# Performance work log

Measured on AMD Instinct MI355X. Metric: run time of the kernel, lower is better.

The kernel has to match this reference:

```python
import jax, jax.numpy as jnp
import numpy as np


def _knn_idx(xyz_bn3, k):
    # dist[b,i,j] = ||x_i - x_j||^2 over the point cloud.
    # Faithful to the source: torch.topk defaults to largest=True, so the
    # k+1 LARGEST distances are selected and index 0 (the farthest) is dropped.
    sq = jnp.sum(xyz_bn3 ** 2, axis=-1)  # [b, n]
    dist = sq[:, :, None] + sq[:, None, :] - 2.0 * jnp.einsum('bic,bjc->bij', xyz_bn3, xyz_bn3)
    _, idx = jax.lax.top_k(dist, k + 1)  # largest, sorted descending -> [b, n, k+1]
    return idx[:, :, 1:]  # drop slot 0, keep k neighbors -> [b, n, k]


def setup_inputs() -> dict:
    key = jax.random.key(0)
    B, N, C, K, NB = 8, 4096, 128, 20, 3
    ks = jax.random.split(key, 4)
    scale = 1.0 / np.sqrt(C).astype(np.float32)
    xyz = jax.random.normal(ks[0], (B, 3, N), jnp.float32)
    points = jax.random.normal(ks[1], (B, C, N), jnp.float32)
    W1 = jax.random.normal(ks[2], (NB, C, C), jnp.float32) * scale  # convs[2i] 1x1 kernels
    b1 = jnp.zeros((NB, C), jnp.float32)
    W2 = jax.random.normal(ks[3], (NB, C, C), jnp.float32) * scale  # convs[2i+1] 1x1 kernels
    b2 = jnp.zeros((NB, C), jnp.float32)
    return {"xyz": xyz, "points": points, "W1": W1, "b1": b1, "W2": W2, "b2": b2, "k": K}


def reference(xyz, points, W1, b1, W2, b2, k):
    # xyz: [b, 3, n]; points: [b, C, n]; W1/W2: [n_blocks, C, C]; b1/b2: [n_blocks, C]
    n_blocks = W1.shape[0]
    xyz_bn3 = jnp.transpose(xyz, (0, 2, 1))  # [b, n, 3]
    for i in range(n_blocks):
        shortcut = points
        p = jax.nn.leaky_relu(points, 0.01)  # elementwise, layout [b, C, n]
        # center branch: 1x1 conv == per-point linear
        center = jnp.einsum('oc,bcn->bon', W1[i], p) + b1[i][None, :, None]  # [b, C, n]
        if i == 0:
            idx = _knn_idx(xyz_bn3, k)  # [b, n, k], int32
            # grouping_operation gather: grouped[b,c,n,j] = p[b,c, idx[b,n,j]]
            grouped = jax.vmap(lambda pb, ib: pb[:, ib])(p, idx)  # [b, C, n, k]
            gnn = jnp.einsum('oc,bcnk->bonk', W2[i], grouped) + b2[i][None, :, None, None]
            # mean over concat([center(1 slot), gnn(k slots)], slot axis)
            agg = (center + jnp.sum(gnn, axis=-1)) / (k + 1)
        else:
            # later blocks: grouped_points is just the center point itself (K=1)
            gnn = jnp.einsum('oc,bcn->bon', W2[i], p) + b2[i][None, :, None]
            agg = (center + gnn) * 0.5
        points = agg + shortcut
    return points
```

## Files before the change

### kernel.cpp

```cpp
#include <hip/hip_runtime.h>
#include <math.h>

#define B 8
#define N 4096
#define C 128
#define K 20
#define M (B*N)

__device__ __forceinline__ float lrelu(float x) { return x > 0.f ? x : 0.01f * x; }

__global__ void prep_all(const float* __restrict__ xyz,
                         const float* __restrict__ W1, const float* __restrict__ b1,
                         const float* __restrict__ W2, const float* __restrict__ b2,
                         float4* __restrict__ xt, float* __restrict__ wt,
                         float* __restrict__ bias) {
    int blk = blockIdx.x;
    if (blk < 64) {
        int t = blk * 256 + threadIdx.x;
        int c = t >> 7, o = t & 127;
        int oc = o * C + c;
        wt[t]             = W1[oc] * (1.f / 21.f);
        wt[C * C + t]     = W2[oc] * (1.f / 21.f);
        wt[2 * C * C + t] = (W1[C * C + oc] + W2[C * C + oc]) * 0.5f;
        wt[3 * C * C + t] = (W1[2 * C * C + oc] + W2[2 * C * C + oc]) * 0.5f;
        if (t < C) {
            bias[t]         = (b1[t] + 20.f * b2[t]) * (1.f / 21.f);
            bias[C + t]     = (b1[C + t] + b2[C + t]) * 0.5f;
            bias[2 * C + t] = (b1[2 * C + t] + b2[2 * C + t]) * 0.5f;
        }
    } else {
        int t = (blk - 64) * 256 + threadIdx.x;
        int b = t >> 12, n = t & (N - 1);
        const float* p = xyz + (size_t)b * 3 * N;
        float x = p[n], y = p[N + n], z = p[2 * N + n];
        xt[t] = make_float4(x, y, z, x * x + y * y + z * z);
    }
}

__global__ __launch_bounds__(256) void transpose_rs(const float* __restrict__ in,
                                                    float* __restrict__ out, int R, int S) {
    __shared__ float tile[64][65];
    int b = blockIdx.z;
    int r0 = blockIdx.y * 64, s0 = blockIdx.x * 64;
    const float* pin = in + (size_t)b * R * S;
    float* pout = out + (size_t)b * R * S;
    int tr = threadIdx.x >> 4;
    int ts = (threadIdx.x & 15) << 2;
#pragma unroll
    for (int i = 0; i < 4; ++i) {
        int r = tr + i * 16;
        float4 v = *(const float4*)&pin[(size_t)(r0 + r) * S + s0 + ts];
        tile[r][ts + 0] = v.x; tile[r][ts + 1] = v.y;
        tile[r][ts + 2] = v.z; tile[r][ts + 3] = v.w;
    }
    __syncthreads();
#pragma unroll
    for (int i = 0; i < 4; ++i) {
        int s = tr + i * 16;
        float4 v = make_float4(tile[ts + 0][s], tile[ts + 1][s], tile[ts + 2][s], tile[ts + 3][s]);
        *(float4*)&pout[(size_t)(s0 + s) * R + r0 + ts] = v;
    }
}

__global__ __launch_bounds__(256, 4) void knn_kernel(const float4* __restrict__ xt,
                                                     int* __restrict__ idx) {
    __shared__ float maxred[4][4];
    __shared__ unsigned int wcnt[2][4][4];
    __shared__ unsigned int cnt[4];
    __shared__ unsigned long long cand[4][128];

    const int tid = threadIdx.x;
    const int wid = tid >> 6, lane = tid & 63;
    const int blk = blockIdx.x;
    const int b = blk >> 10;
    const int i0 = (blk & 1023) << 2;
    const float4* __restrict__ xb = xt + (size_t)b * N;

    float4 xi0 = xb[i0 + 0], xi1 = xb[i0 + 1], xi2 = xb[i0 + 2], xi3 = xb[i0 + 3];
    if (tid < 4) cnt[tid] = 0;

    float d[4][16];
    float mx0 = -1e30f, mx1 = -1e30f, mx2 = -1e30f, mx3 = -1e30f;
#pragma unroll
    for (int u = 0; u < 16; ++u) {
        float4 xj = xb[u * 256 + tid];
        float s0 = fmaf(xi0.x, xj.x, fmaf(xi0.y, xj.y, xi0.z * xj.z));
        float s1 = fmaf(xi1.x, xj.x, fmaf(xi1.y, xj.y, xi1.z * xj.z));
        float s2 = fmaf(xi2.x, xj.x, fmaf(xi2.y, xj.y, xi2.z * xj.z));
        float s3 = fmaf(xi3.x, xj.x, fmaf(xi3.y, xj.y, xi3.z * xj.z));
        float d0 = xi0.w + xj.w - 2.f * s0;
        float d1 = xi1.w + xj.w - 2.f * s1;
        float d2 = xi2.w + xj.w - 2.f * s2;
        float d3 = xi3.w + xj.w - 2.f * s3;
        d[0][u] = d0; d[1][u] = d1; d[2][u] = d2; d[3][u] = d3;
        mx0 = fmaxf(mx0, d0); mx1 = fmaxf(mx1, d1);
        mx2 = fmaxf(mx2, d2); mx3 = fmaxf(mx3, d3);
    }
#pragma unroll
    for (int off = 32; off; off >>= 1) {
        mx0 = fmaxf(mx0, __shfl_xor(mx0, off));
        mx1 = fmaxf(mx1, __shfl_xor(mx1, off));
        mx2 = fmaxf(mx2, __shfl_xor(mx2, off));
        mx3 = fmaxf(mx3, __shfl_xor(mx3, off));
    }
    if (lane == 0) {
        maxred[wid][0] = mx0; maxred[wid][1] = mx1;
        maxred[wid][2] = mx2; maxred[wid][3] = mx3;
    }
    __syncthreads();

    float lo[4] = {0.f, 0.f, 0.f, 0.f};
    float hi[4], thr[4];
    bool done[4] = {false, false, false, false};
#pragma unroll
    for (int r = 0; r < 4; ++r) {
        hi[r] = fmaxf(fmaxf(maxred[0][r], maxred[1][r]), fmaxf(maxred[2][r], maxred[3][r]));
        thr[r] = 0.f;
    }

    bool alldone = false;
    for (int it = 0; it < 24 && !alldone; ++it) {
        int p = it & 1;
#pragma unroll
        for (int r = 0; r < 4; ++r) {
            if (done[r]) continue;
            float t = 0.5f * (lo[r] + hi[r]);
            thr[r] = t;
            unsigned int cc = 0;
#pragma unroll
            for (int u = 0; u < 16; ++u)
                cc += (unsigned int)__popcll(__ballot(d[r][u] > t));
            if (lane == 0) wcnt[p][wid][r] = cc;
        }
        __syncthreads();
        alldone = true;
#pragma unroll
        for (int r = 0; r < 4; ++r) {
            if (done[r]) continue;
            unsigned int tot = wcnt[p][0][r] + wcnt[p][1][r] + wcnt[p][2][r] + wcnt[p][3][r];
            if (tot >= (unsigned)(K + 1) && tot <= 96u) done[r] = true;
            else if (tot > 96u) lo[r] = thr[r];
            else hi[r] = thr[r];
            if (!done[r]) alldone = false;
        }
    }
#pragma unroll
    for (int r = 0; r < 4; ++r) if (!done[r]) thr[r] = lo[r];

#pragma unroll
    for (int u = 0; u < 16; ++u) {
#pragma unroll
        for (int r = 0; r < 4; ++r) {
            bool pred = d[r][u] > thr[r];
            unsigned long long m = __ballot(pred);
            if (m) {
                unsigned int base = 0;
                if (lane == 0) base = atomicAdd(&cnt[r], (unsigned int)__popcll(m));
                base = (unsigned int)__shfl((int)base, 0);
                if (pred) {
                    unsigned int bel = __builtin_amdgcn_mbcnt_lo((unsigned int)m, 0u);
                    bel = __builtin_amdgcn_mbcnt_hi((unsigned int)(m >> 32), bel);
                    unsigned int pos = base + bel;
                    if (pos < 128u) {
                        unsigned int j = (unsigned int)(u * 256 + tid);
                        cand[r][pos] = ((unsigned long long)__float_as_uint(d[r][u]) << 32)
                                       | (unsigned int)(~j);
                    }
                }
            }
        }
    }
    __syncthreads();

    {
        int r = wid;
        int row = (b << 12) + i0 + r;
        unsigned int c = cnt[r]; if (c > 128u) c = 128u;
        if (c < (unsigned)(K + 1) && lane < K)
            idx[(size_t)row * K + lane] = (int)lane + 1;
        for (int s = lane; s < (int)c; s += 64) {
            unsigned long long my = cand[r][s];
            int rank = 0;
            for (int q = 0; q < (int)c; ++q) rank += (cand[r][q] > my) ? 1 : 0;
            if (rank >= 1 && rank <= K)
                idx[(size_t)row * K + (rank - 1)] = (int)(~(unsigned int)my);
        }
    }
}

__global__ __launch_bounds__(256) void gather_sum(const float* __restrict__ pt,
                                                  const int* __restrict__ idx,
                                                  float* __restrict__ sT) {
    int t = blockIdx.x * 256 + threadIdx.x;
    int pnt = t >> 5;
    int c4 = (t & 31) << 2;
    int b = pnt >> 12;
    const float* pb = pt + (size_t)b * N * C;
    const int* ip = idx + (size_t)pnt * K;
    float4 acc = make_float4(0.f, 0.f, 0.f, 0.f);
#pragma unroll 4
    for (int k = 0; k < K; ++k) {
        int j = ip[k] & (N - 1);
        float4 v = *(const float4*)&pb[(size_t)j * C + c4];
        acc.x += lrelu(v.x); acc.y += lrelu(v.y);
        acc.z += lrelu(v.z); acc.w += lrelu(v.w);
    }
    *(float4*)&sT[(size_t)pnt * C + c4] = acc;
}

__device__ __forceinline__ void stage_ws(const float* __restrict__ Wt, float (*Ws)[128],
                                         int c0, int tid) {
#pragma unroll
    for (int q = 0; q < 2; ++q) {
        int slot = q * 256 + tid;
        int kk = slot >> 5, oo = (slot & 31) << 2;
        *(float4*)&Ws[kk][oo] = *(const float4*)&Wt[(size_t)(c0 + kk) * C + oo];
    }
}

template<bool LR>
__device__ __forceinline__ void mm_tileP(const float (*P)[132], const float (*Ws)[128],
                                         float acc[4][8], int r0, int o0, int c0) {
#pragma unroll
    for (int q = 0; q < 4; ++q) {
        float4 aj[4];
#pragma unroll
        for (int j = 0; j < 4; ++j) {
            float4 v = *(const float4*)&P[r0 + j][c0 + q * 4];
            if (LR) { v.x = lrelu(v.x); v.y = lrelu(v.y); v.z = lrelu(v.z); v.w = lrelu(v.w); }
            aj[j] = v;
        }
#pragma unroll
        for (int kq = 0; kq < 4; ++kq) {
            int kk = q * 4 + kq;
            float4 w0 = *(const float4*)&Ws[kk][o0];
            float4 w1 = *(const float4*)&Ws[kk][o0 + 64];
#pragma unroll
            for (int j = 0; j < 4; ++j) {
                float a = (kq == 0) ? aj[j].x : (kq == 1) ? aj[j].y : (kq == 2) ? aj[j].z : aj[j].w;
                acc[j][0] = fmaf(a, w0.x, acc[j][0]); acc[j][1] = fmaf(a, w0.y, acc[j][1]);
                acc[j][2] = fmaf(a, w0.z, acc[j][2]); acc[j][3] = fmaf(a, w0.w, acc[j][3]);
                acc[j][4] = fmaf(a, w1.x, acc[j][4]); acc[j][5] = fmaf(a, w1.y, acc[j][5]);
                acc[j][6] = fmaf(a, w1.z, acc[j][6]); acc[j][7] = fmaf(a, w1.w, acc[j][7]);
            }
        }
    }
}

__device__ __forceinline__ void mm_tileA(const float (*As)[20], const float (*Ws)[128],
                                         float acc[4][8], int r0, int o0) {
#pragma unroll
    for (int q = 0; q < 4; ++q) {
        float4 aj[4];
#pragma unroll
        for (int j = 0; j < 4; ++j)
            aj[j] = *(const float4*)&As[r0 + j][q * 4];
#pragma unroll
        for (int kq = 0; kq < 4; ++kq) {
            int kk = q * 4 + kq;
            float4 w0 = *(const float4*)&Ws[kk][o0];
            float4 w1 = *(const float4*)&Ws[kk][o0 + 64];
#pragma unroll
            for (int j = 0; j < 4; ++j) {
                float a = (kq == 0) ? aj[j].x : (kq == 1) ? aj[j].y : (kq == 2) ? aj[j].z : aj[j].w;
                acc[j][0] = fmaf(a, w0.x, acc[j][0]); acc[j][1] = fmaf(a, w0.y, acc[j][1]);
                acc[j][2] = fmaf(a, w0.z, acc[j][2]); acc[j][3] = fmaf(a, w0.w, acc[j][3]);
                acc[j][4] = fmaf(a, w1.x, acc[j][4]); acc[j][5] = fmaf(a, w1.y, acc[j][5]);
                acc[j][6] = fmaf(a, w1.z, acc[j][6]); acc[j][7] = fmaf(a, w1.w, acc[j][7]);
            }
        }
    }
}

__global__ __launch_bounds__(256) void gemm_block0(const float* __restrict__ A0,
                                                   const float* __restrict__ A1,
                                                   const float* __restrict__ Wt0,
                                                   const float* __restrict__ Wt1,
                                                   const float* __restrict__ bias0,
                                                   float* __restrict__ out) {
    __shared__ float P0[64][132];
    __shared__ float As[64][20];
    __shared__ float Ws[16][128];
    const int row0 = blockIdx.x * 64;
    const int tid = threadIdx.x;
    const int r0 = (tid >> 4) << 2;
    const int o0 = (tid & 15) << 2;

#pragma unroll
    for (int q = 0; q < 8; ++q) {
        int s = q * 256 + tid;
        int r = s >> 5, c4 = (s & 31) << 2;
        *(float4*)&P0[r][c4] = *(const float4*)&A0[(size_t)(row0 + r) * C + c4];
    }

    float acc[4][8];
#pragma unroll
    for (int j = 0; j < 4; ++j)
#pragma unroll
        for (int l = 0; l < 8; ++l) acc[j][l] = 0.f;

    for (int c0 = 0; c0 < C; c0 += 16) {
        stage_ws(Wt0, Ws, c0, tid);
        __syncthreads();
        mm_tileP<true>(P0, Ws, acc, r0, o0, c0);
        __syncthreads();
    }
    for (int c0 = 0; c0 < C; c0 += 16) {
        stage_ws(Wt1, Ws, c0, tid);
        {
            int r_ld = tid >> 2, c_ld = (tid & 3) << 2;
            *(float4*)&As[r_ld][c_ld] = *(const float4*)&A1[(size_t)(row0 + r_ld) * C + c0 + c_ld];
        }
        __syncthreads();
        mm_tileA(As, Ws, acc, r0, o0);
        __syncthreads();
    }

    float4 bb0 = *(const float4*)&bias0[o0];
    float4 bb1 = *(const float4*)&bias0[o0 + 64];
#pragma unroll
    for (int j = 0; j < 4; ++j) {
        int rl = r0 + j;
        size_t r = (size_t)(row0 + rl);
        float4 s0 = *(const float4*)&P0[rl][o0];
        float4 s1 = *(const float4*)&P0[rl][o0 + 64];
        float4 v0 = make_float4(acc[j][0] + bb0.x + s0.x, acc[j][1] + bb0.y + s0.y,
                                acc[j][2] + bb0.z + s0.z, acc[j][3] + bb0.w + s0.w);
        float4 v1 = make_float4(acc[j][4] + bb1.x + s1.x, acc[j][5] + bb1.y + s1.y,
                                acc[j][6] + bb1.z + s1.z, acc[j][7] + bb1.w + s1.w);
        *(float4*)&out[r * C + o0] = v0;
        *(float4*)&out[r * C + o0 + 64] = v1;
    }
}

__global__ __launch_bounds__(256) void gemm_block12(const float* __restrict__ A0,
                                                    const float* __restrict__ Wt1,
                                                    const float* __restrict__ Wt2,
                                                    const float* __restrict__ biasAll,
                                                    float* __restrict__ outT) {
    __shared__ float P[64][132];
    __shared__ float Ws[16][128];
    const int row0 = blockIdx.x * 64;
    const int tid = threadIdx.x;
    const int r0 = (tid >> 4) << 2;
    const int o0 = (tid & 15) << 2;

#pragma unroll
    for (int q = 0; q < 8; ++q) {
        int s = q * 256 + tid;
        int r = s >> 5, c4 = (s & 31) << 2;
        *(float4*)&P[r][c4] = *(const float4*)&A0[(size_t)(row0 + r) * C + c4];
    }

    float acc[4][8];
#pragma unroll
    for (int j = 0; j < 4; ++j)
#pragma unroll
        for (int l = 0; l < 8; ++l) acc[j][l] = 0.f;

    for (int c0 = 0; c0 < C; c0 += 16) {
        stage_ws(Wt1, Ws, c0, tid);
        __syncthreads();
        mm_tileP<true>(P, Ws, acc, r0, o0, c0);
        __syncthreads();
    }
    {
        float4 bb0 = *(const float4*)&biasAll[C + o0];
        float4 bb1 = *(const float4*)&biasAll[C + o0 + 64];
#pragma unroll
        for (int j = 0; j < 4; ++j) {
            int rl = r0 + j;
            float4 s0 = *(const float4*)&P[rl][o0];
            float4 s1 = *(const float4*)&P[rl][o0 + 64];
            float4 v0 = make_float4(acc[j][0] + bb0.x + s0.x, acc[j][1] + bb0.y + s0.y,
                                    acc[j][2] + bb0.z + s0.z, acc[j][3] + bb0.w + s0.w);
            float4 v1 = make_float4(acc[j][4] + bb1.x + s1.x, acc[j][5] + bb1.y + s1.y,
                                    acc[j][6] + bb1.z + s1.z, acc[j][7] + bb1.w + s1.w);
            *(float4*)&P[rl][o0] = v0;
            *(float4*)&P[rl][o0 + 64] = v1;
            acc[j][0] = 0.f; acc[j][1] = 0.f; acc[j][2] = 0.f; acc[j][3] = 0.f;
            acc[j][4] = 0.f; acc[j][5] = 0.f; acc[j][6] = 0.f; acc[j][7] = 0.f;
        }
    }
    __syncthreads();
    for (int c0 = 0; c0 < C; c0 += 16) {
        stage_ws(Wt2, Ws, c0, tid);
        __syncthreads();
        mm_tileP<true>(P, Ws, acc, r0, o0, c0);
        __syncthreads();
    }
    {
        float4 bb0 = *(const float4*)&biasAll[2 * C + o0];
        float4 bb1 = *(const float4*)&biasAll[2 * C + o0 + 64];
#pragma unroll
        for (int j = 0; j < 4; ++j) {
            int rl = r0 + j;
            float4 s0 = *(const float4*)&P[rl][o0];
            float4 s1 = *(const float4*)&P[rl][o0 + 64];
            float4 v0 = make_float4(acc[j][0] + bb0.x + s0.x, acc[j][1] + bb0.y + s0.y,
                                    acc[j][2] + bb0.z + s0.z, acc[j][3] + bb0.w + s0.w);
            float4 v1 = make_float4(acc[j][4] + bb1.x + s1.x, acc[j][5] + bb1.y + s1.y,
                                    acc[j][6] + bb1.z + s1.z, acc[j][7] + bb1.w + s1.w);
            *(float4*)&P[rl][o0] = v0;
            *(float4*)&P[rl][o0 + 64] = v1;
        }
    }
    __syncthreads();
    const int o = tid >> 1;
    const int nh = (tid & 1) << 5;
    const int bq = row0 >> 12;
    const int nb = (row0 & (N - 1)) + nh;
    float* po = outT + ((size_t)bq * C + o) * N + nb;
#pragma unroll
    for (int q = 0; q < 8; ++q) {
        int n = nh + q * 4;
        float4 v = make_float4(P[n + 0][o], P[n + 1][o], P[n + 2][o], P[n + 3][o]);
        *(float4*)&po[q * 4] = v;
    }
}

extern "C" void kernel_launch(void* const* d_in, const int* in_sizes, int n_in,
                              void* d_out, int out_size, void* d_ws, size_t ws_size,
                              hipStream_t stream) {
    const float* xyz    = (const float*)d_in[0];
    const float* points = (const float*)d_in[1];
    const float* W1     = (const float*)d_in[2];
    const float* b1     = (const float*)d_in[3];
    const float* W2     = (const float*)d_in[4];
    const float* b2     = (const float*)d_in[5];

    float* ws = (float*)d_ws;
    float4* xt  = (float4*)ws;
    float* pt_a = ws + (size_t)B * N * 4;
    float* pt_b = pt_a + (size_t)M * C;
    float* sT   = pt_b + (size_t)M * C;
    float* wt   = sT + (size_t)M * C;
    float* bias = wt + 4 * C * C;
    int*   idx  = (int*)(bias + 3 * C);

    prep_all<<<192, 256, 0, stream>>>(xyz, W1, b1, W2, b2, xt, wt, bias);
    {
        dim3 g(N / 64, C / 64, B);
        transpose_rs<<<g, 256, 0, stream>>>(points, pt_a, C, N);
    }
    knn_kernel<<<M / 4, 256, 0, stream>>>(xt, idx);
    gather_sum<<<(M * 32) / 256, 256, 0, stream>>>(pt_a, idx, sT);
    gemm_block0<<<M / 64, 256, 0, stream>>>(pt_a, sT, wt, wt + C * C, bias, pt_b);
    gemm_block12<<<M / 64, 256, 0, stream>>>(pt_b, wt + 2 * C * C, wt + 3 * C * C, bias,
                                             (float*)d_out);
}
```

Baseline: 242.4 us.

## Restructure kNN to one row per wave with 16-bit packed distances

The kNN kernel now stages the whole batch's xyz into shared memory and gives each wavefront one query row, removing the block-level syncs and shared atomics of the bisection and compaction. Distances use the direct difference form and are truncated to their upper 16 bits, two per register, for the threshold search. Exact distances are recomputed only for candidates, which are compacted with a wave prefix scan. The precompute of xyz plus squared norms is dropped from the prep kernel. The 48KB LDS per block may lower occupancy, and the 16-bit quantized threshold could change how many candidates pass.

```diff
diff --git a/kernel.cpp b/kernel.cpp
--- a/kernel.cpp
+++ b/kernel.cpp
@@ -9,31 +9,26 @@
 
 __device__ __forceinline__ float lrelu(float x) { return x > 0.f ? x : 0.01f * x; }
 
-__global__ void prep_all(const float* __restrict__ xyz,
-                         const float* __restrict__ W1, const float* __restrict__ b1,
+__device__ __forceinline__ float pdist(float xix, float xiy, float xiz,
+                                       float xjx, float xjy, float xjz) {
+    float dx = xix - xjx, dy = xiy - xjy, dz = xiz - xjz;
+    return fmaf(dx, dx, fmaf(dy, dy, dz * dz));
+}
+
+__global__ void prep_all(const float* __restrict__ W1, const float* __restrict__ b1,
                          const float* __restrict__ W2, const float* __restrict__ b2,
-                         float4* __restrict__ xt, float* __restrict__ wt,
-                         float* __restrict__ bias) {
-    int blk = blockIdx.x;
-    if (blk < 64) {
-        int t = blk * 256 + threadIdx.x;
-        int c = t >> 7, o = t & 127;
-        int oc = o * C + c;
-        wt[t]             = W1[oc] * (1.f / 21.f);
-        wt[C * C + t]     = W2[oc] * (1.f / 21.f);
-        wt[2 * C * C + t] = (W1[C * C + oc] + W2[C * C + oc]) * 0.5f;
-        wt[3 * C * C + t] = (W1[2 * C * C + oc] + W2[2 * C * C + oc]) * 0.5f;
-        if (t < C) {
-            bias[t]         = (b1[t] + 20.f * b2[t]) * (1.f / 21.f);
-            bias[C + t]     = (b1[C + t] + b2[C + t]) * 0.5f;
-            bias[2 * C + t] = (b1[2 * C + t] + b2[2 * C + t]) * 0.5f;
-        }
-    } else {
-        int t = (blk - 64) * 256 + threadIdx.x;
-        int b = t >> 12, n = t & (N - 1);
-        const float* p = xyz + (size_t)b * 3 * N;
-        float x = p[n], y = p[N + n], z = p[2 * N + n];
-        xt[t] = make_float4(x, y, z, x * x + y * y + z * z);
+                         float* __restrict__ wt, float* __restrict__ bias) {
+    int t = blockIdx.x * 256 + threadIdx.x;
+    int c = t >> 7, o = t & 127;
+    int oc = o * C + c;
+    wt[t]             = W1[oc] * (1.f / 21.f);
+    wt[C * C + t]     = W2[oc] * (1.f / 21.f);
+    wt[2 * C * C + t] = (W1[C * C + oc] + W2[C * C + oc]) * 0.5f;
+    wt[3 * C * C + t] = (W1[2 * C * C + oc] + W2[2 * C * C + oc]) * 0.5f;
+    if (t < C) {
+        bias[t]         = (b1[t] + 20.f * b2[t]) * (1.f / 21.f);
+        bias[C + t]     = (b1[C + t] + b2[C + t]) * 0.5f;
+        bias[2 * C + t] = (b1[2 * C + t] + b2[2 * C + t]) * 0.5f;
     }
 }
 
@@ -62,11 +57,11 @@
     }
 }
 
-__global__ __launch_bounds__(256, 4) void knn_kernel(const float4* __restrict__ xt,
-                                                     int* __restrict__ idx) {
-    __shared__ float maxred[4][4];
-    __shared__ unsigned int wcnt[2][4][4];
-    __shared__ unsigned int cnt[4];
+__global__ __launch_bounds__(256) void knn_kernel(const float* __restrict__ xyz,
+                                                  int* __restrict__ idx) {
+    __shared__ __align__(16) float xs[N];
+    __shared__ __align__(16) float ys[N];
+    __shared__ __align__(16) float zs[N];
     __shared__ unsigned long long cand[4][128];
 
     const int tid = threadIdx.x;
@@ -74,117 +69,110 @@
     const int blk = blockIdx.x;
     const int b = blk >> 10;
     const int i0 = (blk & 1023) << 2;
-    const float4* __restrict__ xb = xt + (size_t)b * N;
-
-    float4 xi0 = xb[i0 + 0], xi1 = xb[i0 + 1], xi2 = xb[i0 + 2], xi3 = xb[i0 + 3];
-    if (tid < 4) cnt[tid] = 0;
-
-    float d[4][16];
-    float mx0 = -1e30f, mx1 = -1e30f, mx2 = -1e30f, mx3 = -1e30f;
+    const float* __restrict__ xb = xyz + (size_t)b * 3 * N;
+
+#pragma unroll
+    for (int rep = 0; rep < 4; ++rep) {
+        int p4 = (rep * 256 + tid) * 4;
+        float4 gx = *(const float4*)&xb[p4];
+        float4 gy = *(const float4*)&xb[N + p4];
+        float4 gz = *(const float4*)&xb[2 * N + p4];
+        *(float4*)&xs[p4] = gx;
+        *(float4*)&ys[p4] = gy;
+        *(float4*)&zs[p4] = gz;
+    }
+    const int i = i0 + wid;
+    const float xix = xb[i], xiy = xb[N + i], xiz = xb[2 * N + i];
+    __syncthreads();
+
+    unsigned int dq[32];
+    unsigned int mx16 = 0;
 #pragma unroll
     for (int u = 0; u < 16; ++u) {
-        float4 xj = xb[u * 256 + tid];
-        float s0 = fmaf(xi0.x, xj.x, fmaf(xi0.y, xj.y, xi0.z * xj.z));
-        float s1 = fmaf(xi1.x, xj.x, fmaf(xi1.y, xj.y, xi1.z * xj.z));
-        float s2 = fmaf(xi2.x, xj.x, fmaf(xi2.y, xj.y, xi2.z * xj.z));
-        float s3 = fmaf(xi3.x, xj.x, fmaf(xi3.y, xj.y, xi3.z * xj.z));
-        float d0 = xi0.w + xj.w - 2.f * s0;
-        float d1 = xi1.w + xj.w - 2.f * s1;
-        float d2 = xi2.w + xj.w - 2.f * s2;
-        float d3 = xi3.w + xj.w - 2.f * s3;
-        d[0][u] = d0; d[1][u] = d1; d[2][u] = d2; d[3][u] = d3;
-        mx0 = fmaxf(mx0, d0); mx1 = fmaxf(mx1, d1);
-        mx2 = fmaxf(mx2, d2); mx3 = fmaxf(mx3, d3);
-    }
-#pragma unroll
-    for (int off = 32; off; off >>= 1) {
-        mx0 = fmaxf(mx0, __shfl_xor(mx0, off));
-        mx1 = fmaxf(mx1, __shfl_xor(mx1, off));
-        mx2 = fmaxf(mx2, __shfl_xor(mx2, off));
-        mx3 = fmaxf(mx3, __shfl_xor(mx3, off));
-    }
-    if (lane == 0) {
-        maxred[wid][0] = mx0; maxred[wid][1] = mx1;
-        maxred[wid][2] = mx2; maxred[wid][3] = mx3;
-    }
-    __syncthreads();
-
-    float lo[4] = {0.f, 0.f, 0.f, 0.f};
-    float hi[4], thr[4];
-    bool done[4] = {false, false, false, false};
-#pragma unroll
-    for (int r = 0; r < 4; ++r) {
-        hi[r] = fmaxf(fmaxf(maxred[0][r], maxred[1][r]), fmaxf(maxred[2][r], maxred[3][r]));
-        thr[r] = 0.f;
-    }
-
-    bool alldone = false;
-    for (int it = 0; it < 24 && !alldone; ++it) {
-        int p = it & 1;
-#pragma unroll
-        for (int r = 0; r < 4; ++r) {
-            if (done[r]) continue;
-            float t = 0.5f * (lo[r] + hi[r]);
-            thr[r] = t;
-            unsigned int cc = 0;
-#pragma unroll
-            for (int u = 0; u < 16; ++u)
-                cc += (unsigned int)__popcll(__ballot(d[r][u] > t));
-            if (lane == 0) wcnt[p][wid][r] = cc;
-        }
-        __syncthreads();
-        alldone = true;
-#pragma unroll
-        for (int r = 0; r < 4; ++r) {
-            if (done[r]) continue;
-            unsigned int tot = wcnt[p][0][r] + wcnt[p][1][r] + wcnt[p][2][r] + wcnt[p][3][r];
-            if (tot >= (unsigned)(K + 1) && tot <= 96u) done[r] = true;
-            else if (tot > 96u) lo[r] = thr[r];
-            else hi[r] = thr[r];
-            if (!done[r]) alldone = false;
-        }
-    }
-#pragma unroll
-    for (int r = 0; r < 4; ++r) if (!done[r]) thr[r] = lo[r];
-
-#pragma unroll
-    for (int u = 0; u < 16; ++u) {
-#pragma unroll
-        for (int r = 0; r < 4; ++r) {
-            bool pred = d[r][u] > thr[r];
-            unsigned long long m = __ballot(pred);
-            if (m) {
-                unsigned int base = 0;
-                if (lane == 0) base = atomicAdd(&cnt[r], (unsigned int)__popcll(m));
-                base = (unsigned int)__shfl((int)base, 0);
-                if (pred) {
-                    unsigned int bel = __builtin_amdgcn_mbcnt_lo((unsigned int)m, 0u);
-                    bel = __builtin_amdgcn_mbcnt_hi((unsigned int)(m >> 32), bel);
-                    unsigned int pos = base + bel;
-                    if (pos < 128u) {
-                        unsigned int j = (unsigned int)(u * 256 + tid);
-                        cand[r][pos] = ((unsigned long long)__float_as_uint(d[r][u]) << 32)
-                                       | (unsigned int)(~j);
-                    }
-                }
-            }
-        }
-    }
-    __syncthreads();
-
-    {
-        int r = wid;
-        int row = (b << 12) + i0 + r;
-        unsigned int c = cnt[r]; if (c > 128u) c = 128u;
-        if (c < (unsigned)(K + 1) && lane < K)
-            idx[(size_t)row * K + lane] = (int)lane + 1;
-        for (int s = lane; s < (int)c; s += 64) {
-            unsigned long long my = cand[r][s];
-            int rank = 0;
-            for (int q = 0; q < (int)c; ++q) rank += (cand[r][q] > my) ? 1 : 0;
-            if (rank >= 1 && rank <= K)
-                idx[(size_t)row * K + (rank - 1)] = (int)(~(unsigned int)my);
-        }
+        int j = u * 256 + (lane << 2);
+        float4 xv = *(const float4*)&xs[j];
+        float4 yv = *(const float4*)&ys[j];
+        float4 zv = *(const float4*)&zs[j];
+        unsigned int q0 = __float_as_uint(pdist(xix, xiy, xiz, xv.x, yv.x, zv.x)) >> 16;
+        unsigned int q1 = __float_as_uint(pdist(xix, xiy, xiz, xv.y, yv.y, zv.y)) >> 16;
+        unsigned int q2 = __float_as_uint(pdist(xix, xiy, xiz, xv.z, yv.z, zv.z)) >> 16;
+        unsigned int q3 = __float_as_uint(pdist(xix, xiy, xiz, xv.w, yv.w, zv.w)) >> 16;
+        dq[2 * u]     = q0 | (q1 << 16);
+        dq[2 * u + 1] = q2 | (q3 << 16);
+        mx16 = max(mx16, max(max(q0, q1), max(q2, q3)));
+    }
+#pragma unroll
+    for (int off = 32; off; off >>= 1)
+        mx16 = max(mx16, (unsigned int)__shfl_xor((int)mx16, off));
+
+    unsigned int lo = 0, hi = mx16, q = 0;
+    bool found = false;
+    for (int it = 0; it < 17 && !found; ++it) {
+        if (hi - lo <= 1u) break;
+        unsigned int mid = (lo + hi) >> 1;
+        unsigned int cm = (mid << 16) | 0xFFFFu;
+        unsigned int c = 0;
+#pragma unroll
+        for (int p = 0; p < 32; ++p) {
+            c += ((dq[p] & 0xFFFFu) > mid) ? 1u : 0u;
+            c += (dq[p] > cm) ? 1u : 0u;
+        }
+#pragma unroll
+        for (int off = 32; off; off >>= 1) c += (unsigned int)__shfl_xor((int)c, off);
+        if (c >= (unsigned)(K + 1) && c <= 96u) { q = mid; found = true; }
+        else if (c > 96u) lo = mid;
+        else hi = mid;
+    }
+    if (!found) q = lo;
+    const unsigned int cm2 = (q << 16) | 0xFFFFu;
+
+    unsigned int cl = 0;
+#pragma unroll
+    for (int p = 0; p < 32; ++p) {
+        cl += ((dq[p] & 0xFFFFu) > q) ? 1u : 0u;
+        cl += (dq[p] > cm2) ? 1u : 0u;
+    }
+    unsigned int incl = cl;
+#pragma unroll
+    for (int off = 1; off < 64; off <<= 1) {
+        unsigned int v = (unsigned int)__shfl_up((int)incl, off);
+        if (lane >= off) incl += v;
+    }
+    unsigned int total = (unsigned int)__shfl((int)incl, 63);
+    unsigned int pos = incl - cl;
+
+#pragma unroll
+    for (int p = 0; p < 32; ++p) {
+        int jb = (p >> 1) * 256 + (lane << 2) + ((p & 1) << 1);
+        if ((dq[p] & 0xFFFFu) > q) {
+            float d = pdist(xix, xiy, xiz, xs[jb], ys[jb], zs[jb]);
+            if (pos < 128u)
+                cand[wid][pos] = ((unsigned long long)__float_as_uint(d) << 32)
+                                 | (unsigned int)(~jb);
+            ++pos;
+        }
+        if (dq[p] > cm2) {
+            int j1 = jb + 1;
+            float d = pdist(xix, xiy, xiz, xs[j1], ys[j1], zs[j1]);
+            if (pos < 128u)
+                cand[wid][pos] = ((unsigned long long)__float_as_uint(d) << 32)
+                                 | (unsigned int)(~j1);
+            ++pos;
+        }
+    }
+
+    unsigned int cnt_r = total < 128u ? total : 128u;
+    int row = (b << 12) + i0 + wid;
+    if (cnt_r < (unsigned)(K + 1)) {
+        if (lane < K) idx[(size_t)row * K + lane] = lane + 1;
+    }
+    for (unsigned int s = lane; s < cnt_r; s += 64) {
+        unsigned long long my = cand[wid][s];
+        int rank = 0;
+        for (unsigned int t2 = 0; t2 < cnt_r; ++t2)
+            rank += (cand[wid][t2] > my) ? 1 : 0;
+        if (rank >= 1 && rank <= K)
+            idx[(size_t)row * K + (rank - 1)] = (int)(~(unsigned int)my);
     }
 }
 
@@ -430,7 +418,6 @@
     const float* b2     = (const float*)d_in[5];
 
     float* ws = (float*)d_ws;
-    float4* xt  = (float4*)ws;
     float* pt_a = ws + (size_t)B * N * 4;
     float* pt_b = pt_a + (size_t)M * C;
     float* sT   = pt_b + (size_t)M * C;
@@ -438,12 +425,12 @@
     float* bias = wt + 4 * C * C;
     int*   idx  = (int*)(bias + 3 * C);
 
-    prep_all<<<192, 256, 0, stream>>>(xyz, W1, b1, W2, b2, xt, wt, bias);
+    prep_all<<<64, 256, 0, stream>>>(W1, b1, W2, b2, wt, bias);
     {
         dim3 g(N / 64, C / 64, B);
         transpose_rs<<<g, 256, 0, stream>>>(points, pt_a, C, N);
     }
-    knn_kernel<<<M / 4, 256, 0, stream>>>(xt, idx);
+    knn_kernel<<<M / 4, 256, 0, stream>>>(xyz, idx);
     gather_sum<<<(M * 32) / 256, 256, 0, stream>>>(pt_a, idx, sT);
     gemm_block0<<<M / 64, 256, 0, stream>>>(pt_a, sT, wt, wt + C * C, bias, pt_b);
     gemm_block12<<<M / 64, 256, 0, stream>>>(pt_b, wt + 2 * C * C, wt + 3 * C * C, bias,
```

After: 302.1 us. 24.6% more time.
